# Kernel tuning notes

Hardware: AMD Instinct MI355X
Metric: run time of the kernel (lower is better)

## Reference

```python
import jax, jax.numpy as jnp
import numpy as np

B, C, H, W = 8, 512, 32, 32
HEADS = 8
DIM = C // HEADS
EPS = 1e-5


def setup_inputs() -> dict:
    key = jax.random.key(0)
    ks = jax.random.split(key, 7)
    scale = 1.0 / np.sqrt(C)
    return {
        "x": jax.random.normal(ks[0], (B, C, H, W), dtype=jnp.float32),
        "gn_gamma": jnp.ones((C,), dtype=jnp.float32),
        "gn_beta": jnp.zeros((C,), dtype=jnp.float32),
        "w_qkv": jax.random.normal(ks[1], (3 * HEADS * DIM, C), dtype=jnp.float32) * scale,
        "b_qkv": jax.random.normal(ks[2], (3 * HEADS * DIM,), dtype=jnp.float32) * 0.01,
        "w_proj": jax.random.normal(ks[3], (C, HEADS * DIM), dtype=jnp.float32) * scale,
        "b_proj": jax.random.normal(ks[4], (C,), dtype=jnp.float32) * 0.01,
    }


def reference(x, gn_gamma, gn_beta, w_qkv, b_qkv, w_proj, b_proj):
    b, c, h, w = x.shape
    n = h * w
    # GroupNorm with 1 group: normalize over (C,H,W) per sample (biased var)
    mu = jnp.mean(x, axis=(1, 2, 3), keepdims=True)
    var = jnp.var(x, axis=(1, 2, 3), keepdims=True)
    xn = (x - mu) * jax.lax.rsqrt(var + EPS)
    xn = xn * gn_gamma[None, :, None, None] + gn_beta[None, :, None, None]
    # 1x1 conv QKV projection == channel matmul
    qkv = jnp.einsum('bchw,oc->bohw', xn, w_qkv) + b_qkv[None, :, None, None]
    qkv = qkv.reshape(b, 3, HEADS, DIM, n)  # matches view(B,3*heads,dim,N).chunk(3,dim=1)
    q, k, v = qkv[:, 0], qkv[:, 1], qkv[:, 2]  # each (B, heads, dim, N)
    # scale uses full channel count C, as in the source (C ** -0.5)
    dot = jnp.einsum('bhdn,bhdm->bhnm', q, k) * (c ** -0.5)
    attn = jax.nn.softmax(dot, axis=-1)
    vals = jnp.einsum('bhnm,bhdm->bhdn', attn, v)  # (B, heads, dim, N)
    vals = vals.reshape(b, HEADS * DIM, h, w)
    return jnp.einsum('bchw,oc->bohw', vals, w_proj) + b_proj[None, :, None, None]
```

## Files before the change

kernel.cpp:

```cpp
#include <hip/hip_runtime.h>
#include <hip/hip_bf16.h>
#include <math.h>

#define NB 8
#define NC 512
#define NN 1024
#define NHEADS 8
#define EPSV 1e-5f
#define SC2F 0.06376351307f

typedef __attribute__((ext_vector_type(8))) short bf16x8;
typedef __attribute__((ext_vector_type(4))) short bf16x4;
typedef __attribute__((ext_vector_type(4))) float f32x4;
typedef __attribute__((ext_vector_type(16))) float f32x16;

#define MFMA16(a,b,c) __builtin_amdgcn_mfma_f32_16x16x32_bf16(a,b,c,0,0,0)
#define MFMA32(a,b,c) __builtin_amdgcn_mfma_f32_32x32x16_bf16(a,b,c,0,0,0)

static __device__ __forceinline__ short f2bf(float f) {
    __hip_bfloat16 h = __float2bfloat16(f);
    return *reinterpret_cast<short*>(&h);
}

static __device__ __forceinline__ unsigned cvt_pk_bf16(float lo, float hi) {
    unsigned r;
    asm("v_cvt_pk_bf16_f32 %0, %1, %2" : "=v"(r) : "v"(lo), "v"(hi));
    return r;
}

static __device__ __forceinline__ void gload16(const void* g, void* l) {
    __builtin_amdgcn_global_load_lds((const __attribute__((address_space(1))) void*)g,
                                     (__attribute__((address_space(3))) void*)l, 16, 0, 0);
}

#define WS_PART_SUM 0
#define WS_PART_SQ  1024
#define WS_XNT   4096
#define WS_QT    (WS_XNT  + 2097152)
#define WS_KT    (WS_QT   + 2097152)
#define WS_V     (WS_KT   + 2097152)
#define WS_VALST (WS_V    + 2097152)
#define WS_WQB   (WS_VALST+ 2097152)
#define WS_WPB   (WS_WQB  + 393216)

__global__ __launch_bounds__(256) void prep_kernel(const float* __restrict__ x,
                                                   const float* __restrict__ wq,
                                                   const float* __restrict__ wp,
                                                   float* __restrict__ ws) {
    int blk = blockIdx.x;
    if (blk < 512) {
        int b = blk >> 6;
        int s = blk & 63;
        const float* xb = x + (size_t)b * (NC * NN) + (size_t)s * 8192;
        float sum = 0.f, sq = 0.f;
        for (int i = threadIdx.x; i < 2048; i += 256) {
            float4 v = ((const float4*)xb)[i];
            sum += v.x + v.y + v.z + v.w;
            sq  += v.x*v.x + v.y*v.y + v.z*v.z + v.w*v.w;
        }
        #pragma unroll
        for (int off = 32; off; off >>= 1) {
            sum += __shfl_down(sum, off);
            sq  += __shfl_down(sq,  off);
        }
        __shared__ float s1[4], s2[4];
        int wave = threadIdx.x >> 6, lane = threadIdx.x & 63;
        if (lane == 0) { s1[wave] = sum; s2[wave] = sq; }
        __syncthreads();
        if (threadIdx.x == 0) {
            float a = 0.f, c2 = 0.f;
            #pragma unroll
            for (int w = 0; w < 4; w++) { a += s1[w]; c2 += s2[w]; }
            ws[WS_PART_SUM + b*64 + s] = a;
            ws[WS_PART_SQ  + b*64 + s] = c2;
        }
    } else {
        int i = (blk - 512) * 256 + threadIdx.x;
        const float* s;
        __hip_bfloat16* d;
        if (i < 196608) { s = wq; d = (__hip_bfloat16*)(ws + WS_WQB); }
        else            { s = wp; d = (__hip_bfloat16*)(ws + WS_WPB); i -= 196608; }
        float4 v = ((const float4*)s)[i];
        bf16x4 w;
        w[0] = f2bf(v.x); w[1] = f2bf(v.y); w[2] = f2bf(v.z); w[3] = f2bf(v.w);
        *(bf16x4*)(d + (size_t)i*4) = w;
    }
}

__global__ __launch_bounds__(256) void normalize_t(const float* __restrict__ x,
                                                   const float* __restrict__ gamma,
                                                   const float* __restrict__ beta,
                                                   const float* __restrict__ ws,
                                                   __hip_bfloat16* __restrict__ xnT) {
    int nt = blockIdx.x & 15, ct = (blockIdx.x >> 4) & 7, b = blockIdx.x >> 7;
    __shared__ __hip_bfloat16 tb[64][72];
    float s = 0.f, q = 0.f;
    const float4* ps = (const float4*)(ws + WS_PART_SUM + b*64);
    const float4* pq = (const float4*)(ws + WS_PART_SQ  + b*64);
    #pragma unroll
    for (int i = 0; i < 16; i++) {
        float4 a = ps[i]; s += a.x + a.y + a.z + a.w;
        float4 c = pq[i]; q += c.x + c.y + c.z + c.w;
    }
    const float inv = 1.f / (float)(NC * NN);
    float mu   = s * inv;
    float var  = q * inv - mu * mu;
    float rstd = rsqrtf(var + EPSV);

    const float* xb = x + ((size_t)b*512 + ct*64)*1024 + nt*64;
    int t = threadIdx.x;
    int cl = t >> 4, n4 = (t & 15) * 4;
    #pragma unroll
    for (int i = 0; i < 4; i++) {
        int c = i*16 + cl;
        float gm = gamma[ct*64 + c];
        float g = gm * rstd;
        float be = beta[ct*64 + c] - mu * g;
        float4 v = *(const float4*)(xb + (size_t)c*1024 + n4);
        tb[n4+0][c] = __float2bfloat16(v.x*g + be);
        tb[n4+1][c] = __float2bfloat16(v.y*g + be);
        tb[n4+2][c] = __float2bfloat16(v.z*g + be);
        tb[n4+3][c] = __float2bfloat16(v.w*g + be);
    }
    __syncthreads();
    #pragma unroll
    for (int i = 0; i < 2; i++) {
        int idx = i*256 + t;
        int n = idx >> 3, c8 = (idx & 7) * 8;
        *(bf16x8*)(xnT + ((size_t)b*1024 + nt*64 + n)*512 + ct*64 + c8) =
            *(const bf16x8*)&tb[n][c8];
    }
}

template<int OT, int MODE>
__global__ __launch_bounds__(256) void gemm_mfma(const __hip_bfloat16* __restrict__ Aw,
                                                 const __hip_bfloat16* __restrict__ Bx,
                                                 const float* __restrict__ bias,
                                                 float* __restrict__ Yout,
                                                 __hip_bfloat16* __restrict__ QTx,
                                                 __hip_bfloat16* __restrict__ KTx,
                                                 __hip_bfloat16* __restrict__ Vx) {
    __shared__ __align__(16) __hip_bfloat16 lds_raw[17408];
    const int bx = blockIdx.x;
    const int swz = (bx & 7) * (OT * 8) + (bx >> 3);
    const int nt = swz & 7;
    const int ot = (swz >> 3) % OT;
    const int bb = swz / (8 * OT);
    const int o0 = ot * 128, n0 = nt * 128;

    const int t = threadIdx.x, wv = t >> 6, l = t & 63;
    const int lr = l & 31, lh = l >> 5;
    const int wr = wv >> 1, wc = wv & 1;

    const __hip_bfloat16* Ag = Aw + (size_t)o0 * 512;
    const __hip_bfloat16* Bg = Bx + ((size_t)bb * 1024 + n0) * 512;
    __hip_bfloat16* Ab = lds_raw;
    __hip_bfloat16* Bb = lds_raw + 128*64;

    f32x16 acc[2][2];
    #pragma unroll
    for (int a1 = 0; a1 < 2; a1++)
        #pragma unroll
        for (int a2 = 0; a2 < 2; a2++)
            #pragma unroll
            for (int r = 0; r < 16; r++) acc[a1][a2][r] = 0.f;

    const int srow = wv*8 + (l >> 3);
    const int sblk = (l & 7) ^ (l >> 3);

    for (int k0 = 0; k0 < 512; k0 += 64) {
        __syncthreads();
        #pragma unroll
        for (int c = 0; c < 4; c++) {
            int row = c*32 + srow;
            gload16(Ag + (size_t)row*512 + k0 + sblk*8, Ab + (c*32 + wv*8)*64);
            gload16(Bg + (size_t)row*512 + k0 + sblk*8, Bb + (c*32 + wv*8)*64);
        }
        __syncthreads();
        #pragma unroll
        for (int ks = 0; ks < 4; ks++) {
            bf16x8 af[2], bfr[2];
            #pragma unroll
            for (int mi = 0; mi < 2; mi++) {
                int row = wr*64 + mi*32 + lr;
                af[mi] = *(const bf16x8*)(Ab + row*64 + (((ks*2 + lh) ^ (row & 7)) * 8));
            }
            #pragma unroll
            for (int ni = 0; ni < 2; ni++) {
                int row = wc*64 + ni*32 + lr;
                bfr[ni] = *(const bf16x8*)(Bb + row*64 + (((ks*2 + lh) ^ (row & 7)) * 8));
            }
            acc[0][0] = MFMA32(af[0], bfr[0], acc[0][0]);
            acc[0][1] = MFMA32(af[0], bfr[1], acc[0][1]);
            acc[1][0] = MFMA32(af[1], bfr[0], acc[1][0]);
            acc[1][1] = MFMA32(af[1], bfr[1], acc[1][1]);
        }
    }

    if (MODE == 0) {
        #pragma unroll
        for (int mi = 0; mi < 2; mi++)
            #pragma unroll
            for (int q = 0; q < 4; q++) {
                int obase = o0 + wr*64 + mi*32 + 8*q + 4*lh;
                float4 bv = *(const float4*)(bias + obase);
                #pragma unroll
                for (int ni = 0; ni < 2; ni++) {
                    int nn = n0 + wc*64 + ni*32 + lr;
                    #pragma unroll
                    for (int j = 0; j < 4; j++)
                        Yout[((size_t)bb*512 + obase + j)*1024 + nn] = acc[mi][ni][q*4+j] + bv[j];
                }
            }
    } else {
        int sec = o0 >> 9;
        if (sec == 2) {
            int od0 = o0 & 511;
            int mperm = ((lr & 12) << 1) + ((lr & 16) >> 2) + (lr & 3);
            #pragma unroll
            for (int mi = 0; mi < 2; mi++)
                #pragma unroll
                for (int q = 0; q < 4; q++) {
                    int ob = wr*64 + mi*32 + 8*q + 4*lh;
                    float4 bv = *(const float4*)(bias + o0 + ob);
                    #pragma unroll
                    for (int j = 0; j < 4; j++) {
                        int ol = od0 + ob + j;
                        int h = ol >> 6, d = ol & 63;
                        __hip_bfloat16* dst = Vx + ((size_t)((bb<<3) + h)*64 + d)*1024;
                        #pragma unroll
                        for (int ni = 0; ni < 2; ni++) {
                            int nn = n0 + wc*64 + ni*32 + mperm;
                            dst[nn] = __float2bfloat16(acc[mi][ni][q*4+j] + bv[j]);
                        }
                    }
                }
        } else {
            const float qs = (sec == 0) ? SC2F : 1.0f;
            __syncthreads();
            __hip_bfloat16* tb = lds_raw;
            #pragma unroll
            for (int mi = 0; mi < 2; mi++)
                #pragma unroll
                for (int q = 0; q < 4; q++) {
                    int ob = wr*64 + mi*32 + 8*q + 4*lh;
                    float4 bv = *(const float4*)(bias + o0 + ob);
                    #pragma unroll
                    for (int ni = 0; ni < 2; ni++) {
                        int nn = wc*64 + ni*32 + lr;
                        bf16x4 w;
                        #pragma unroll
                        for (int j = 0; j < 4; j++) w[j] = f2bf((acc[mi][ni][q*4+j] + bv[j]) * qs);
                        *(bf16x4*)&tb[(size_t)nn*136 + ob] = w;
                    }
                }
            __syncthreads();
            __hip_bfloat16* dst0 = (sec == 0) ? QTx : KTx;
            int h0 = (o0 & 511) >> 6;
            #pragma unroll
            for (int i = 0; i < 8; i++) {
                int idx = i*256 + t;
                int n = idx >> 4, rem = idx & 15;
                int hh = rem >> 3, slot = rem & 7;
                int hf32 = (slot & 4) << 3;
                int g4   = (slot & 3) << 2;
                bf16x4 lo = *(const bf16x4*)&tb[(size_t)n*136 + hh*64 + hf32 + g4];
                bf16x4 hi = *(const bf16x4*)&tb[(size_t)n*136 + hh*64 + hf32 + 16 + g4];
                bf16x8 w;
                w[0]=lo[0]; w[1]=lo[1]; w[2]=lo[2]; w[3]=lo[3];
                w[4]=hi[0]; w[5]=hi[1]; w[6]=hi[2]; w[7]=hi[3];
                *(bf16x8*)(dst0 + ((size_t)((bb<<3) + h0 + hh)*1024 + n0 + n)*64 + slot*8) = w;
            }
        }
    }
}

__global__ __launch_bounds__(256) void attn_mfma(const __hip_bfloat16* __restrict__ QT,
                                                 const __hip_bfloat16* __restrict__ KT,
                                                 const __hip_bfloat16* __restrict__ Vb,
                                                 __hip_bfloat16* __restrict__ valsT) {
    const int bh = ((blockIdx.x & 7) << 3) | ((blockIdx.x >> 3) & 7);
    const int qt = blockIdx.x >> 6;
    const int t = threadIdx.x;
    const int wv = t >> 6, lane = t & 63;
    const int g = lane >> 4, li = lane & 15;

    const __hip_bfloat16* QTg = QT + (size_t)bh * NN * 64;
    const __hip_bfloat16* KTg = KT + (size_t)bh * NN * 64;
    const __hip_bfloat16* Vg  = Vb + (size_t)bh * 64 * NN;

    __shared__ __align__(16) __hip_bfloat16 k_ls[2*4096];
    __shared__ __align__(16) __hip_bfloat16 v_ls[2*4096];

    const int nq0 = qt*64 + wv*16;

    bf16x8 qf[2];
    {
        const __hip_bfloat16* qp = QTg + (size_t)(nq0 + li) * 64;
        qf[0] = *(const bf16x8*)(qp + 8*g);
        qf[1] = *(const bf16x8*)(qp + 32 + 8*g);
    }

    bf16x8 onesf;
    #pragma unroll
    for (int j = 0; j < 8; j++) onesf[j] = (short)0x3F80;

    float m_run = -1e30f;
    f32x4 o_acc[4], o_l;
    #pragma unroll
    for (int dt = 0; dt < 4; dt++) { o_acc[dt][0]=0.f; o_acc[dt][1]=0.f; o_acc[dt][2]=0.f; o_acc[dt][3]=0.f; }
    o_l[0]=0.f; o_l[1]=0.f; o_l[2]=0.f; o_l[3]=0.f;

    auto STAGE = [&](int buf, int ck) {
        const int mc0 = ck * 64;
        __hip_bfloat16* kb = k_ls + buf*4096;
        __hip_bfloat16* vb = v_ls + buf*4096;
        #pragma unroll
        for (int p = 0; p < 2; p++) {
            int idx = t + p*256;
            int row = idx >> 3, sl = idx & 7;
            int sk = sl ^ (row & 7);
            gload16(KTg + (size_t)(mc0+row)*64 + sk*8, kb + idx*8);
            gload16(Vg + (size_t)row*NN + mc0 + sk*8, vb + idx*8);
        }
    };

    STAGE(0, 0);
    __syncthreads();
    int cur = 0;

    for (int ck = 0; ck < 16; ck++) {
        if (ck < 15) STAGE(cur ^ 1, ck + 1);

        const __hip_bfloat16* kb = k_ls + cur*4096;
        const __hip_bfloat16* vb = v_ls + cur*4096;

        f32x4 s_acc[4];
        __builtin_amdgcn_s_setprio(1);
        #pragma unroll
        for (int mt = 0; mt < 4; mt++) {
            f32x4 c; c[0]=0.f; c[1]=0.f; c[2]=0.f; c[3]=0.f;
            #pragma unroll
            for (int hf = 0; hf < 2; hf++) {
                int row = mt*16 + li;
                int sl = ((hf<<2) + g) ^ (li & 7);
                bf16x8 kf = *(const bf16x8*)(kb + row*64 + sl*8);
                c = MFMA16(kf, qf[hf], c);
            }
            s_acc[mt] = c;
        }
        __builtin_amdgcn_s_setprio(0);

        float cmax = fmaxf(s_acc[0][0], s_acc[0][1]);
        cmax = fmaxf(fmaxf(cmax, s_acc[0][2]), s_acc[0][3]);
        cmax = fmaxf(fmaxf(cmax, s_acc[1][0]), s_acc[1][1]);
        cmax = fmaxf(fmaxf(cmax, s_acc[1][2]), s_acc[1][3]);
        cmax = fmaxf(fmaxf(cmax, s_acc[2][0]), s_acc[2][1]);
        cmax = fmaxf(fmaxf(cmax, s_acc[2][2]), s_acc[2][3]);
        cmax = fmaxf(fmaxf(cmax, s_acc[3][0]), s_acc[3][1]);
        cmax = fmaxf(fmaxf(cmax, s_acc[3][2]), s_acc[3][3]);
        cmax = fmaxf(cmax, __shfl_xor(cmax, 16));
        cmax = fmaxf(cmax, __shfl_xor(cmax, 32));
        if (!__all(cmax <= m_run + 8.0f)) {
            float m_new = fmaxf(m_run, cmax);
            float resc = __builtin_amdgcn_exp2f(m_run - m_new);
            f32x4 rv;
            #pragma unroll
            for (int r = 0; r < 4; r++) rv[r] = __shfl(resc, 4*g + r);
            #pragma unroll
            for (int dt = 0; dt < 4; dt++) {
                o_acc[dt][0]*=rv[0]; o_acc[dt][1]*=rv[1]; o_acc[dt][2]*=rv[2]; o_acc[dt][3]*=rv[3];
            }
            o_l[0]*=rv[0]; o_l[1]*=rv[1]; o_l[2]*=rv[2]; o_l[3]*=rv[3];
            m_run = m_new;
        }

        bf16x8 pf[2];
        #pragma unroll
        for (int ks = 0; ks < 2; ks++) {
            union { bf16x8 v; unsigned u[4]; } pk;
            #pragma unroll
            for (int d4 = 0; d4 < 4; d4++) {
                const int i0 = 8*ks + 2*d4, i1 = i0 + 1;
                float e0 = __builtin_amdgcn_exp2f(s_acc[i0>>2][i0&3] - m_run);
                float e1 = __builtin_amdgcn_exp2f(s_acc[i1>>2][i1&3] - m_run);
                pk.u[d4] = cvt_pk_bf16(e0, e1);
            }
            pf[ks] = pk.v;
        }

        __builtin_amdgcn_s_setprio(1);
        #pragma unroll
        for (int dt = 0; dt < 4; dt++) {
            #pragma unroll
            for (int ks = 0; ks < 2; ks++) {
                int row = dt*16 + li;
                int sl = ((ks<<2) + g) ^ (li & 7);
                bf16x8 vf = *(const bf16x8*)(vb + row*64 + sl*8);
                o_acc[dt] = MFMA16(pf[ks], vf, o_acc[dt]);
            }
        }
        o_l = MFMA16(pf[0], onesf, o_l);
        o_l = MFMA16(pf[1], onesf, o_l);
        __builtin_amdgcn_s_setprio(0);

        __syncthreads();
        cur ^= 1;
    }

    f32x4 lv;
    #pragma unroll
    for (int r = 0; r < 4; r++) lv[r] = 1.0f / o_l[r];
    const int bI = bh >> 3, hI = bh & 7;
    __hip_bfloat16* vt = valsT + (size_t)bI*1024*512 + hI*64;
    #pragma unroll
    for (int dt = 0; dt < 4; dt++)
        #pragma unroll
        for (int r = 0; r < 4; r++)
            vt[(size_t)(nq0 + 4*g + r)*512 + dt*16 + li] = __float2bfloat16(o_acc[dt][r]*lv[r]);
}

extern "C" void kernel_launch(void* const* d_in, const int* in_sizes, int n_in,
                              void* d_out, int out_size, void* d_ws, size_t ws_size,
                              hipStream_t stream) {
    const float* x      = (const float*)d_in[0];
    const float* gamma  = (const float*)d_in[1];
    const float* beta   = (const float*)d_in[2];
    const float* w_qkv  = (const float*)d_in[3];
    const float* b_qkv  = (const float*)d_in[4];
    const float* w_proj = (const float*)d_in[5];
    const float* b_proj = (const float*)d_in[6];
    float* ws   = (float*)d_ws;
    float* out  = (float*)d_out;
    __hip_bfloat16* xnT   = (__hip_bfloat16*)(ws + WS_XNT);
    __hip_bfloat16* QT    = (__hip_bfloat16*)(ws + WS_QT);
    __hip_bfloat16* KT    = (__hip_bfloat16*)(ws + WS_KT);
    __hip_bfloat16* Vx    = (__hip_bfloat16*)(ws + WS_V);
    __hip_bfloat16* valsT = (__hip_bfloat16*)(ws + WS_VALST);
    __hip_bfloat16* wqb   = (__hip_bfloat16*)(ws + WS_WQB);
    __hip_bfloat16* wpb   = (__hip_bfloat16*)(ws + WS_WPB);

    prep_kernel<<<dim3(1536), dim3(256), 0, stream>>>(x, w_qkv, w_proj, ws);
    normalize_t<<<dim3(1024), dim3(256), 0, stream>>>(x, gamma, beta, ws, xnT);
    gemm_mfma<12, 1><<<dim3(768), dim3(256), 0, stream>>>(wqb, xnT, b_qkv,
                                                          nullptr, QT, KT, Vx);
    attn_mfma<<<dim3(1024), dim3(256), 0, stream>>>(QT, KT, Vx, valsT);
    gemm_mfma<4, 0><<<dim3(256), dim3(256), 0, stream>>>(wpb, valsT, b_proj,
                                                         out, nullptr, nullptr, nullptr);
}
```

Measured before the change: 81.69 us.

## Double attention block query tile to 128 and fold max subtraction into MFMA init

```diff
diff --git a/kernel.cpp b/kernel.cpp
--- a/kernel.cpp
+++ b/kernel.cpp
@@ -275,7 +275,7 @@
     }
 }
 
-__global__ __launch_bounds__(256) void attn_mfma(const __hip_bfloat16* __restrict__ QT,
+__global__ __launch_bounds__(512) void attn_mfma(const __hip_bfloat16* __restrict__ QT,
                                                  const __hip_bfloat16* __restrict__ KT,
                                                  const __hip_bfloat16* __restrict__ Vb,
                                                  __hip_bfloat16* __restrict__ valsT) {
@@ -292,7 +292,7 @@
     __shared__ __align__(16) __hip_bfloat16 k_ls[2*4096];
     __shared__ __align__(16) __hip_bfloat16 v_ls[2*4096];
 
-    const int nq0 = qt*64 + wv*16;
+    const int nq0 = qt*128 + wv*16;
 
     bf16x8 qf[2];
     {
@@ -305,7 +305,7 @@
     #pragma unroll
     for (int j = 0; j < 8; j++) onesf[j] = (short)0x3F80;
 
-    float m_run = -1e30f;
+    float m_run = 0.0f;
     f32x4 o_acc[4], o_l;
     #pragma unroll
     for (int dt = 0; dt < 4; dt++) { o_acc[dt][0]=0.f; o_acc[dt][1]=0.f; o_acc[dt][2]=0.f; o_acc[dt][3]=0.f; }
@@ -313,16 +313,10 @@
 
     auto STAGE = [&](int buf, int ck) {
         const int mc0 = ck * 64;
-        __hip_bfloat16* kb = k_ls + buf*4096;
-        __hip_bfloat16* vb = v_ls + buf*4096;
-        #pragma unroll
-        for (int p = 0; p < 2; p++) {
-            int idx = t + p*256;
-            int row = idx >> 3, sl = idx & 7;
-            int sk = sl ^ (row & 7);
-            gload16(KTg + (size_t)(mc0+row)*64 + sk*8, kb + idx*8);
-            gload16(Vg + (size_t)row*NN + mc0 + sk*8, vb + idx*8);
-        }
+        int row = t >> 3, sl = t & 7;
+        int sk = sl ^ (row & 7);
+        gload16(KTg + (size_t)(mc0+row)*64 + sk*8, k_ls + buf*4096 + t*8);
+        gload16(Vg + (size_t)row*NN + mc0 + sk*8, v_ls + buf*4096 + t*8);
     };
 
     STAGE(0, 0);
@@ -335,11 +329,13 @@
         const __hip_bfloat16* kb = k_ls + cur*4096;
         const __hip_bfloat16* vb = v_ls + cur*4096;
 
+        f32x4 cini;
+        cini[0] = -m_run; cini[1] = -m_run; cini[2] = -m_run; cini[3] = -m_run;
         f32x4 s_acc[4];
         __builtin_amdgcn_s_setprio(1);
         #pragma unroll
         for (int mt = 0; mt < 4; mt++) {
-            f32x4 c; c[0]=0.f; c[1]=0.f; c[2]=0.f; c[3]=0.f;
+            f32x4 c = cini;
             #pragma unroll
             for (int hf = 0; hf < 2; hf++) {
                 int row = mt*16 + li;
@@ -361,9 +357,17 @@
         cmax = fmaxf(fmaxf(cmax, s_acc[3][2]), s_acc[3][3]);
         cmax = fmaxf(cmax, __shfl_xor(cmax, 16));
         cmax = fmaxf(cmax, __shfl_xor(cmax, 32));
-        if (!__all(cmax <= m_run + 8.0f)) {
-            float m_new = fmaxf(m_run, cmax);
-            float resc = __builtin_amdgcn_exp2f(m_run - m_new);
+
+        if (ck == 0) {
+            #pragma unroll
+            for (int mt = 0; mt < 4; mt++) {
+                s_acc[mt][0] -= cmax; s_acc[mt][1] -= cmax;
+                s_acc[mt][2] -= cmax; s_acc[mt][3] -= cmax;
+            }
+            m_run = cmax;
+        } else if (!__all(cmax <= 8.0f)) {
+            float d = fmaxf(cmax, 0.0f);
+            float resc = __builtin_amdgcn_exp2f(-d);
             f32x4 rv;
             #pragma unroll
             for (int r = 0; r < 4; r++) rv[r] = __shfl(resc, 4*g + r);
@@ -372,7 +376,12 @@
                 o_acc[dt][0]*=rv[0]; o_acc[dt][1]*=rv[1]; o_acc[dt][2]*=rv[2]; o_acc[dt][3]*=rv[3];
             }
             o_l[0]*=rv[0]; o_l[1]*=rv[1]; o_l[2]*=rv[2]; o_l[3]*=rv[3];
-            m_run = m_new;
+            #pragma unroll
+            for (int mt = 0; mt < 4; mt++) {
+                s_acc[mt][0] -= d; s_acc[mt][1] -= d;
+                s_acc[mt][2] -= d; s_acc[mt][3] -= d;
+            }
+            m_run += d;
         }
 
         bf16x8 pf[2];
@@ -382,8 +391,8 @@
             #pragma unroll
             for (int d4 = 0; d4 < 4; d4++) {
                 const int i0 = 8*ks + 2*d4, i1 = i0 + 1;
-                float e0 = __builtin_amdgcn_exp2f(s_acc[i0>>2][i0&3] - m_run);
-                float e1 = __builtin_amdgcn_exp2f(s_acc[i1>>2][i1&3] - m_run);
+                float e0 = __builtin_amdgcn_exp2f(s_acc[i0>>2][i0&3]);
+                float e1 = __builtin_amdgcn_exp2f(s_acc[i1>>2][i1&3]);
                 pk.u[d4] = cvt_pk_bf16(e0, e1);
             }
             pf[ks] = pk.v;
@@ -444,7 +453,7 @@
     normalize_t<<<dim3(1024), dim3(256), 0, stream>>>(x, gamma, beta, ws, xnT);
     gemm_mfma<12, 1><<<dim3(768), dim3(256), 0, stream>>>(wqb, xnT, b_qkv,
                                                           nullptr, QT, KT, Vx);
-    attn_mfma<<<dim3(1024), dim3(256), 0, stream>>>(QT, KT, Vx, valsT);
+    attn_mfma<<<dim3(512), dim3(512), 0, stream>>>(QT, KT, Vx, valsT);
     gemm_mfma<4, 0><<<dim3(256), dim3(256), 0, stream>>>(wpb, valsT, b_proj,
                                                          out, nullptr, nullptr, nullptr);
 }
```

Result: faster. 73.70 us (-9.8%).
